# Optimization experiments

Hardware: AMD Instinct MI355X
Metric: run time of the kernel (lower is better)

Reference implementation:

```python
import jax, jax.numpy as jnp
import numpy as np

HIDDEN = 1024
HEADS = 16
HEAD_SIZE = HIDDEN // HEADS
N, L = 2, 2048


def setup_inputs() -> dict:
    key = jax.random.key(0)
    ks = jax.random.split(key, 9)
    s = 1.0 / np.sqrt(HIDDEN)
    x = jax.random.normal(ks[0], (N, L, HIDDEN), dtype=jnp.float32)
    Wq = jax.random.normal(ks[1], (HIDDEN, HIDDEN), dtype=jnp.float32) * s
    Wk = jax.random.normal(ks[2], (HIDDEN, HIDDEN), dtype=jnp.float32) * s
    Wv = jax.random.normal(ks[3], (HIDDEN, HIDDEN), dtype=jnp.float32) * s
    Wo = jax.random.normal(ks[4], (HIDDEN, HIDDEN), dtype=jnp.float32) * s
    bq = jax.random.normal(ks[5], (HIDDEN,), dtype=jnp.float32) * s
    bk = jax.random.normal(ks[6], (HIDDEN,), dtype=jnp.float32) * s
    bv = jax.random.normal(ks[7], (HIDDEN,), dtype=jnp.float32) * s
    bo = jax.random.normal(ks[8], (HIDDEN,), dtype=jnp.float32) * s
    return {"x": x, "Wq": Wq, "bq": bq, "Wk": Wk, "bk": bk,
            "Wv": Wv, "bv": bv, "Wo": Wo, "bo": bo}


def reference(x, Wq, bq, Wk, bk, Wv, bv, Wo, bo):
    n, l, _ = x.shape
    # torch Linear: y = x @ W.T + b
    q = (x @ Wq.T + bq).reshape(n, l, HEADS, HEAD_SIZE)
    k = (x @ Wk.T + bk).reshape(n, l, HEADS, HEAD_SIZE)
    v = (x @ Wv.T + bv).reshape(n, l, HEADS, HEAD_SIZE)
    # NOTE: module does NOT apply 1/sqrt(head_size) scaling
    sims = jnp.einsum('nqhs,nkhs->nhqk', q, k)  # (N,H,L,L)
    attn = jax.nn.softmax(sims, axis=-1)
    ctx = jnp.einsum('nhqk,nkhs->nqhs', attn, v).reshape(n, l, HIDDEN)
    return ctx @ Wo.T + bo
```

## Files before the change

### kernel.cpp

```cpp
#include <hip/hip_runtime.h>
#include <stdint.h>
#include <stddef.h>

#define HIDDEN 1024
#define HEADS  16
#define HDIM   64
#define NBATCH 2
#define SEQ    2048
#define TOK    (NBATCH*SEQ)

typedef __attribute__((ext_vector_type(8))) short bf16x8;
typedef __attribute__((ext_vector_type(4))) float f32x4;
typedef unsigned short bf16u;

__device__ __forceinline__ unsigned short f2bf(float f) {
  union { float f; unsigned int u; } c; c.f = f;
  unsigned int u = c.u;
  unsigned int r = (u + 0x7fffu + ((u >> 16) & 1u)) >> 16;
  return (unsigned short)r;
}

__global__ __launch_bounds__(256) void convert_kernel(
    const float* __restrict__ x,
    const float* __restrict__ wq, const float* __restrict__ wk,
    const float* __restrict__ wv, const float* __restrict__ wo,
    bf16u* __restrict__ xb, bf16u* __restrict__ wqkvb, bf16u* __restrict__ wob) {
  const int XG = TOK*HIDDEN/4;
  const int WG = HIDDEN*HIDDEN/4;
  int i = blockIdx.x*blockDim.x + threadIdx.x;
  const float* src; bf16u* dst; int off;
  if (i < XG)            { src = x;  dst = xb;                      off = i; }
  else if (i < XG+WG)    { src = wq; dst = wqkvb;                   off = i-XG; }
  else if (i < XG+2*WG)  { src = wk; dst = wqkvb +   HIDDEN*HIDDEN; off = i-XG-WG; }
  else if (i < XG+3*WG)  { src = wv; dst = wqkvb + 2*HIDDEN*HIDDEN; off = i-XG-2*WG; }
  else if (i < XG+4*WG)  { src = wo; dst = wob;                     off = i-XG-3*WG; }
  else return;
  float4 v = ((const float4*)src)[off];
  ushort4 o;
  o.x = f2bf(v.x); o.y = f2bf(v.y); o.z = f2bf(v.z); o.w = f2bf(v.w);
  *(ushort4*)&dst[(size_t)off*4] = o;
}

__device__ __forceinline__ void gemm_core(const bf16u* __restrict__ Abase,
                                          const bf16u* __restrict__ Bbase,
                                          bf16u* As, bf16u* Bs,
                                          f32x4 (&acc)[4][4]) {
  const int K = HIDDEN;
  const int t = threadIdx.x;
  const int w = t >> 6, lane = t & 63;
  const int wm = (w >> 1) * 64, wn = (w & 1) * 64;
  const int row = lane & 15, kq = (lane >> 4) * 8;
  const int c0 = t, c1 = t + 256;
  const int rA0 = c0 >> 2, k80 = (c0 & 3) * 8;
  const int rA1 = c1 >> 2, k81 = (c1 & 3) * 8;
  bf16u* ldsA0 = As + (size_t)(w*64)*8;
  bf16u* ldsA1 = As + (size_t)(256 + w*64)*8;
  bf16u* ldsB0 = Bs + (size_t)(w*64)*8;
  bf16u* ldsB1 = Bs + (size_t)(256 + w*64)*8;

  for (int k0 = 0; k0 < K; k0 += 32) {
    __builtin_amdgcn_global_load_lds(
        (const __attribute__((address_space(1))) void*)(Abase + (size_t)rA0*K + k0 + k80),
        (__attribute__((address_space(3))) void*)ldsA0, 16, 0, 0);
    __builtin_amdgcn_global_load_lds(
        (const __attribute__((address_space(1))) void*)(Abase + (size_t)rA1*K + k0 + k81),
        (__attribute__((address_space(3))) void*)ldsA1, 16, 0, 0);
    __builtin_amdgcn_global_load_lds(
        (const __attribute__((address_space(1))) void*)(Bbase + (size_t)rA0*K + k0 + k80),
        (__attribute__((address_space(3))) void*)ldsB0, 16, 0, 0);
    __builtin_amdgcn_global_load_lds(
        (const __attribute__((address_space(1))) void*)(Bbase + (size_t)rA1*K + k0 + k81),
        (__attribute__((address_space(3))) void*)ldsB1, 16, 0, 0);
    __syncthreads();
    bf16x8 af[4], bf[4];
    #pragma unroll
    for (int mi = 0; mi < 4; mi++)
      af[mi] = *(const bf16x8*)&As[(wm + mi*16 + row)*32 + kq];
    #pragma unroll
    for (int ni = 0; ni < 4; ni++)
      bf[ni] = *(const bf16x8*)&Bs[(wn + ni*16 + row)*32 + kq];
    #pragma unroll
    for (int mi = 0; mi < 4; mi++)
      #pragma unroll
      for (int ni = 0; ni < 4; ni++)
        acc[mi][ni] = __builtin_amdgcn_mfma_f32_16x16x32_bf16(af[mi], bf[ni], acc[mi][ni], 0, 0, 0);
    __syncthreads();
  }
}

__global__ __launch_bounds__(256) void qkv_kernel(
    const bf16u* __restrict__ xb, const bf16u* __restrict__ wqkvb,
    const float* __restrict__ bq, const float* __restrict__ bk, const float* __restrict__ bv,
    bf16u* __restrict__ qb, bf16u* __restrict__ kb, bf16u* __restrict__ vtb) {
  __shared__ bf16u As[128*32];
  __shared__ bf16u Bs[128*32];
  f32x4 z = {0.f,0.f,0.f,0.f};
  f32x4 acc[4][4];
  #pragma unroll
  for (int i = 0; i < 4; i++)
    #pragma unroll
    for (int j = 0; j < 4; j++) acc[i][j] = z;
  const int n0 = blockIdx.x * 128, m0 = blockIdx.y * 128;
  gemm_core(xb + (size_t)m0*HIDDEN, wqkvb + (size_t)n0*HIDDEN, As, Bs, acc);

  const int t = threadIdx.x, w = t >> 6, lane = t & 63;
  const int wm = (w >> 1) * 64, wn = (w & 1) * 64;
  #pragma unroll
  for (int mi = 0; mi < 4; mi++) {
    #pragma unroll
    for (int ni = 0; ni < 4; ni++) {
      const int col = n0 + wn + ni*16 + (lane & 15);
      const int which = col >> 10, c = col & 1023;
      const int head = c >> 6, d = c & 63;
      const float bias = (which == 0 ? bq : (which == 1 ? bk : bv))[c];
      #pragma unroll
      for (int j = 0; j < 4; j++) {
        const int rowm = m0 + wm + mi*16 + ((lane >> 4) * 4) + j;
        const int n = rowm >> 11, l = rowm & 2047;
        const bf16u hv = f2bf(acc[mi][ni][j] + bias);
        if (which == 0)
          qb[(((size_t)n*HEADS + head)*SEQ + l)*HDIM + d] = hv;
        else if (which == 1)
          kb[(((size_t)n*HEADS + head)*SEQ + l)*HDIM + d] = hv;
        else
          vtb[(((size_t)n*HEADS + head)*HDIM + d)*SEQ + l] = hv;
      }
    }
  }
}

__global__ __launch_bounds__(256) void attn_kernel(
    const bf16u* __restrict__ qb, const bf16u* __restrict__ kb,
    const bf16u* __restrict__ vtb, bf16u* __restrict__ ctxb) {
  __shared__ bf16u Ks[2][64*64];
  __shared__ bf16u Vs[2][64*64];
  __shared__ bf16u Pl[4][16*64];
  const int t = threadIdx.x, w = t >> 6, lane = t & 63;
  const int row = lane & 15, hi = lane >> 4, kq8 = hi * 8;
  const int qt = blockIdx.x, nh = blockIdx.y;
  const int n = nh >> 4, h = nh & 15;
  const bf16u* Qb = qb  + (size_t)nh * SEQ * HDIM;
  const bf16u* Kb = kb  + (size_t)nh * SEQ * HDIM;
  const bf16u* Vt = vtb + (size_t)nh * HDIM * SEQ;

  const int c0 = w*64 + lane, c1 = c0 + 256;
  const int r0 = c0 >> 3, e0 = ((c0 & 7) ^ (r0 & 7)) * 8;
  const int r1 = c1 >> 3, e1 = ((c1 & 7) ^ (r1 & 7)) * 8;

  const int qrow = qt*64 + w*16 + row;
  const bf16x8 aq0 = *(const bf16x8*)&Qb[(size_t)qrow*HDIM + kq8];
  const bf16x8 aq1 = *(const bf16x8*)&Qb[(size_t)qrow*HDIM + 32 + kq8];
  f32x4 z = {0.f,0.f,0.f,0.f};
  float mr[4] = {-1e30f,-1e30f,-1e30f,-1e30f};
  float lr[4] = {0.f,0.f,0.f,0.f};
  f32x4 ao[4] = {z,z,z,z};
  bf16u* P = &Pl[w][0];

  auto stage = [&](int buf, int kv0) {
    __builtin_amdgcn_global_load_lds(
        (const __attribute__((address_space(1))) void*)(Kb + (size_t)(kv0 + r0)*HDIM + e0),
        (__attribute__((address_space(3))) void*)(&Ks[buf][(size_t)(w*64)*8]), 16, 0, 0);
    __builtin_amdgcn_global_load_lds(
        (const __attribute__((address_space(1))) void*)(Kb + (size_t)(kv0 + r1)*HDIM + e1),
        (__attribute__((address_space(3))) void*)(&Ks[buf][(size_t)(256 + w*64)*8]), 16, 0, 0);
    __builtin_amdgcn_global_load_lds(
        (const __attribute__((address_space(1))) void*)(Vt + (size_t)r0*SEQ + kv0 + e0),
        (__attribute__((address_space(3))) void*)(&Vs[buf][(size_t)(w*64)*8]), 16, 0, 0);
    __builtin_amdgcn_global_load_lds(
        (const __attribute__((address_space(1))) void*)(Vt + (size_t)r1*SEQ + kv0 + e1),
        (__attribute__((address_space(3))) void*)(&Vs[buf][(size_t)(256 + w*64)*8]), 16, 0, 0);
  };

  stage(0, 0);
  asm volatile("s_waitcnt vmcnt(0)" ::: "memory");
  __builtin_amdgcn_s_barrier();

  for (int it = 0; it < 32; ++it) {
    const int cur = it & 1;
    if (it < 31) stage(cur ^ 1, (it + 1) * 64);

    f32x4 s[4] = {z,z,z,z};
    bf16x8 bk0[4], bk1[4];
    #pragma unroll
    for (int cb = 0; cb < 4; cb++) {
      const int kvr = cb*16 + row;
      const int sw = kvr & 7;
      bk0[cb] = *(const bf16x8*)&Ks[cur][kvr*64 + ((hi     ^ sw) * 8)];
      bk1[cb] = *(const bf16x8*)&Ks[cur][kvr*64 + (((4+hi) ^ sw) * 8)];
    }
    __builtin_amdgcn_s_setprio(1);
    #pragma unroll
    for (int cb = 0; cb < 4; cb++) {
      s[cb] = __builtin_amdgcn_mfma_f32_16x16x32_bf16(aq0, bk0[cb], s[cb], 0, 0, 0);
      s[cb] = __builtin_amdgcn_mfma_f32_16x16x32_bf16(aq1, bk1[cb], s[cb], 0, 0, 0);
    }
    __builtin_amdgcn_s_setprio(0);

    float tmax[4], rs[4], sc[4], p[4][4];
    #pragma unroll
    for (int j = 0; j < 4; j++)
      tmax[j] = fmaxf(fmaxf(s[0][j], s[1][j]), fmaxf(s[2][j], s[3][j]));
    #pragma unroll
    for (int m = 1; m <= 8; m <<= 1)
      #pragma unroll
      for (int j = 0; j < 4; j++)
        tmax[j] = fmaxf(tmax[j], __shfl_xor(tmax[j], m));
    #pragma unroll
    for (int j = 0; j < 4; j++) {
      float nm = fmaxf(mr[j], tmax[j]);
      sc[j] = __expf(mr[j] - nm);
      mr[j] = nm;
      rs[j] = 0.f;
    }
    #pragma unroll
    for (int cb = 0; cb < 4; cb++)
      #pragma unroll
      for (int j = 0; j < 4; j++) {
        p[cb][j] = __expf(s[cb][j] - mr[j]);
        rs[j] += p[cb][j];
      }
    #pragma unroll
    for (int m = 1; m <= 8; m <<= 1)
      #pragma unroll
      for (int j = 0; j < 4; j++)
        rs[j] += __shfl_xor(rs[j], m);
    #pragma unroll
    for (int j = 0; j < 4; j++)
      lr[j] = lr[j]*sc[j] + rs[j];
    #pragma unroll
    for (int db = 0; db < 4; db++)
      #pragma unroll
      for (int j = 0; j < 4; j++)
        ao[db][j] *= sc[j];

    #pragma unroll
    for (int cb = 0; cb < 4; cb++)
      #pragma unroll
      for (int j = 0; j < 4; j++) {
        const int qr = hi*4 + j;
        P[qr*64 + (((cb*16 + row) ^ ((qr & 7) << 3)))] = f2bf(p[cb][j]);
      }
    asm volatile("s_waitcnt lgkmcnt(0)" ::: "memory");
    __builtin_amdgcn_sched_barrier(0);

    bf16x8 ap[2], bv[2][4];
    #pragma unroll
    for (int ks = 0; ks < 2; ks++) {
      ap[ks] = *(const bf16x8*)&P[row*64 + (((ks*4+hi) ^ (row & 7)) * 8)];
      #pragma unroll
      for (int db = 0; db < 4; db++) {
        const int dr = db*16 + row;
        bv[ks][db] = *(const bf16x8*)&Vs[cur][dr*64 + (((ks*4+hi) ^ (dr & 7)) * 8)];
      }
    }
    __builtin_amdgcn_s_setprio(1);
    #pragma unroll
    for (int ks = 0; ks < 2; ks++)
      #pragma unroll
      for (int db = 0; db < 4; db++)
        ao[db] = __builtin_amdgcn_mfma_f32_16x16x32_bf16(ap[ks], bv[ks][db], ao[db], 0, 0, 0);
    __builtin_amdgcn_s_setprio(0);

    if (it < 31) asm volatile("s_waitcnt vmcnt(0)" ::: "memory");
    __builtin_amdgcn_s_barrier();
  }

  float inv[4];
  #pragma unroll
  for (int j = 0; j < 4; j++) inv[j] = 1.0f / lr[j];
  #pragma unroll
  for (int db = 0; db < 4; db++)
    #pragma unroll
    for (int j = 0; j < 4; j++) {
      const int l = qt*64 + w*16 + (lane >> 4)*4 + j;
      const int d = db*16 + row;
      ctxb[((size_t)n*SEQ + l)*HIDDEN + h*HDIM + d] = f2bf(ao[db][j] * inv[j]);
    }
}

__global__ __launch_bounds__(256) void oproj_kernel(
    const bf16u* __restrict__ ctxb, const bf16u* __restrict__ wob,
    const float* __restrict__ bo, float* __restrict__ out) {
  __shared__ bf16u As[128*32];
  __shared__ bf16u Bs[128*32];
  f32x4 z = {0.f,0.f,0.f,0.f};
  f32x4 acc[4][4];
  #pragma unroll
  for (int i = 0; i < 4; i++)
    #pragma unroll
    for (int j = 0; j < 4; j++) acc[i][j] = z;
  const int n0 = blockIdx.x * 128, m0 = blockIdx.y * 128;
  gemm_core(ctxb + (size_t)m0*HIDDEN, wob + (size_t)n0*HIDDEN, As, Bs, acc);

  const int t = threadIdx.x, w = t >> 6, lane = t & 63;
  const int wm = (w >> 1) * 64, wn = (w & 1) * 64;
  #pragma unroll
  for (int mi = 0; mi < 4; mi++) {
    #pragma unroll
    for (int ni = 0; ni < 4; ni++) {
      const int col = n0 + wn + ni*16 + (lane & 15);
      const float bias = bo[col];
      #pragma unroll
      for (int j = 0; j < 4; j++) {
        const int rowm = m0 + wm + mi*16 + ((lane >> 4)*4) + j;
        out[(size_t)rowm*HIDDEN + col] = acc[mi][ni][j] + bias;
      }
    }
  }
}

extern "C" void kernel_launch(void* const* d_in, const int* in_sizes, int n_in,
                              void* d_out, int out_size, void* d_ws, size_t ws_size,
                              hipStream_t stream) {
  const float* x  = (const float*)d_in[0];
  const float* Wq = (const float*)d_in[1];
  const float* bq = (const float*)d_in[2];
  const float* Wk = (const float*)d_in[3];
  const float* bk = (const float*)d_in[4];
  const float* Wv = (const float*)d_in[5];
  const float* bv = (const float*)d_in[6];
  const float* Wo = (const float*)d_in[7];
  const float* bo = (const float*)d_in[8];
  float* out = (float*)d_out;

  bf16u* xb    = (bf16u*)d_ws;
  bf16u* wqkvb = xb    + (size_t)TOK*HIDDEN;
  bf16u* wob   = wqkvb + (size_t)3*HIDDEN*HIDDEN;
  bf16u* qb    = wob   + (size_t)HIDDEN*HIDDEN;
  bf16u* kb    = qb    + (size_t)TOK*HIDDEN;
  bf16u* vtb   = kb    + (size_t)TOK*HIDDEN;
  bf16u* ctxb  = vtb   + (size_t)TOK*HIDDEN;

  convert_kernel<<<8192, 256, 0, stream>>>(x, Wq, Wk, Wv, Wo, xb, wqkvb, wob);
  qkv_kernel<<<dim3(24, 32), 256, 0, stream>>>(xb, wqkvb, bq, bk, bv, qb, kb, vtb);
  attn_kernel<<<dim3(32, 32), 256, 0, stream>>>(qb, kb, vtb, ctxb);
  oproj_kernel<<<dim3(8, 32), 256, 0, stream>>>(ctxb, wob, bo, out);
}
```

Before: 277.8 us.

## Transpose QK^T MFMA so each lane owns one query row; skip rescale when max unchanged

Swaps the MFMA operands so the score tile comes out transposed, with each lane holding one query row. The row max and row sum then need only two cross-lane shuffles instead of four per value, and the softmax state shrinks to a scalar per lane. Rescaling of the output accumulator is skipped when no row max rises across the wave, and P is written to LDS as packed 8-byte bf16 stores using the library conversion. The gains come from fewer shuffles and LDS stores, at the cost of a divergent branch and extra shuffles to redistribute the scale factors to the output layout.

Measured after the change: 246.3 us. -11.3%, faster.

```diff
diff --git a/kernel.cpp b/kernel.cpp
--- a/kernel.cpp
+++ b/kernel.cpp
@@ -1,4 +1,5 @@
 #include <hip/hip_runtime.h>
+#include <hip/hip_bf16.h>
 #include <stdint.h>
 #include <stddef.h>
 
@@ -18,6 +19,14 @@
   unsigned int u = c.u;
   unsigned int r = (u + 0x7fffu + ((u >> 16) & 1u)) >> 16;
   return (unsigned short)r;
+}
+
+__device__ __forceinline__ unsigned int pk2bf(float a, float b) {
+  __hip_bfloat16 ba = __float2bfloat16(a), bb = __float2bfloat16(b);
+  unsigned short ua, ub;
+  __builtin_memcpy(&ua, &ba, 2);
+  __builtin_memcpy(&ub, &bb, 2);
+  return (unsigned int)ua | ((unsigned int)ub << 16);
 }
 
 __global__ __launch_bounds__(256) void convert_kernel(
@@ -151,8 +160,8 @@
   const bf16x8 aq0 = *(const bf16x8*)&Qb[(size_t)qrow*HDIM + kq8];
   const bf16x8 aq1 = *(const bf16x8*)&Qb[(size_t)qrow*HDIM + 32 + kq8];
   f32x4 z = {0.f,0.f,0.f,0.f};
-  float mr[4] = {-1e30f,-1e30f,-1e30f,-1e30f};
-  float lr[4] = {0.f,0.f,0.f,0.f};
+  float mr = -1e30f;
+  float lr = 0.f;
   f32x4 ao[4] = {z,z,z,z};
   bf16u* P = &Pl[w][0];
 
@@ -179,7 +188,7 @@
     const int cur = it & 1;
     if (it < 31) stage(cur ^ 1, (it + 1) * 64);
 
-    f32x4 s[4] = {z,z,z,z};
+    f32x4 s[4];
     bf16x8 bk0[4], bk1[4];
     #pragma unroll
     for (int cb = 0; cb < 4; cb++) {
@@ -191,55 +200,57 @@
     __builtin_amdgcn_s_setprio(1);
     #pragma unroll
     for (int cb = 0; cb < 4; cb++) {
-      s[cb] = __builtin_amdgcn_mfma_f32_16x16x32_bf16(aq0, bk0[cb], s[cb], 0, 0, 0);
-      s[cb] = __builtin_amdgcn_mfma_f32_16x16x32_bf16(aq1, bk1[cb], s[cb], 0, 0, 0);
+      s[cb] = __builtin_amdgcn_mfma_f32_16x16x32_bf16(bk0[cb], aq0, z, 0, 0, 0);
+      s[cb] = __builtin_amdgcn_mfma_f32_16x16x32_bf16(bk1[cb], aq1, s[cb], 0, 0, 0);
     }
     __builtin_amdgcn_s_setprio(0);
 
-    float tmax[4], rs[4], sc[4], p[4][4];
-    #pragma unroll
-    for (int j = 0; j < 4; j++)
-      tmax[j] = fmaxf(fmaxf(s[0][j], s[1][j]), fmaxf(s[2][j], s[3][j]));
-    #pragma unroll
-    for (int m = 1; m <= 8; m <<= 1)
+    float pm = s[0][0];
+    #pragma unroll
+    for (int cb = 0; cb < 4; cb++)
       #pragma unroll
       for (int j = 0; j < 4; j++)
-        tmax[j] = fmaxf(tmax[j], __shfl_xor(tmax[j], m));
-    #pragma unroll
-    for (int j = 0; j < 4; j++) {
-      float nm = fmaxf(mr[j], tmax[j]);
-      sc[j] = __expf(mr[j] - nm);
-      mr[j] = nm;
-      rs[j] = 0.f;
-    }
+        pm = fmaxf(pm, s[cb][j]);
+    pm = fmaxf(pm, __shfl_xor(pm, 16));
+    pm = fmaxf(pm, __shfl_xor(pm, 32));
+
+    if (!__all(pm <= mr)) {
+      const float nm = fmaxf(mr, pm);
+      const float sc = __expf(mr - nm);
+      mr = nm;
+      lr *= sc;
+      float scj[4];
+      #pragma unroll
+      for (int j = 0; j < 4; j++)
+        scj[j] = __shfl(sc, hi*4 + j);
+      #pragma unroll
+      for (int db = 0; db < 4; db++)
+        #pragma unroll
+        for (int j = 0; j < 4; j++)
+          ao[db][j] *= scj[j];
+    }
+
+    float p[4][4];
+    float rs = 0.f;
     #pragma unroll
     for (int cb = 0; cb < 4; cb++)
       #pragma unroll
       for (int j = 0; j < 4; j++) {
-        p[cb][j] = __expf(s[cb][j] - mr[j]);
-        rs[j] += p[cb][j];
+        p[cb][j] = __expf(s[cb][j] - mr);
+        rs += p[cb][j];
       }
-    #pragma unroll
-    for (int m = 1; m <= 8; m <<= 1)
-      #pragma unroll
-      for (int j = 0; j < 4; j++)
-        rs[j] += __shfl_xor(rs[j], m);
-    #pragma unroll
-    for (int j = 0; j < 4; j++)
-      lr[j] = lr[j]*sc[j] + rs[j];
-    #pragma unroll
-    for (int db = 0; db < 4; db++)
-      #pragma unroll
-      for (int j = 0; j < 4; j++)
-        ao[db][j] *= sc[j];
-
-    #pragma unroll
-    for (int cb = 0; cb < 4; cb++)
-      #pragma unroll
-      for (int j = 0; j < 4; j++) {
-        const int qr = hi*4 + j;
-        P[qr*64 + (((cb*16 + row) ^ ((qr & 7) << 3)))] = f2bf(p[cb][j]);
-      }
+    rs += __shfl_xor(rs, 16);
+    rs += __shfl_xor(rs, 32);
+    lr += rs;
+
+    #pragma unroll
+    for (int cb = 0; cb < 4; cb++) {
+      uint2 pk;
+      pk.x = pk2bf(p[cb][0], p[cb][1]);
+      pk.y = pk2bf(p[cb][2], p[cb][3]);
+      const int slot = cb*2 + (hi >> 1);
+      *(uint2*)&P[row*64 + ((slot ^ (row & 7)) * 8) + (hi & 1)*4] = pk;
+    }
     asm volatile("s_waitcnt lgkmcnt(0)" ::: "memory");
     __builtin_amdgcn_sched_barrier(0);
 
@@ -265,16 +276,18 @@
     __builtin_amdgcn_s_barrier();
   }
 
-  float inv[4];
-  #pragma unroll
-  for (int j = 0; j < 4; j++) inv[j] = 1.0f / lr[j];
+  const float linv = 1.0f / lr;
+  float invj[4];
+  #pragma unroll
+  for (int j = 0; j < 4; j++)
+    invj[j] = __shfl(linv, hi*4 + j);
   #pragma unroll
   for (int db = 0; db < 4; db++)
     #pragma unroll
     for (int j = 0; j < 4; j++) {
-      const int l = qt*64 + w*16 + (lane >> 4)*4 + j;
+      const int l = qt*64 + w*16 + hi*4 + j;
       const int d = db*16 + row;
-      ctxb[((size_t)n*SEQ + l)*HIDDEN + h*HDIM + d] = f2bf(ao[db][j] * inv[j]);
+      ctxb[((size_t)n*SEQ + l)*HIDDEN + h*HDIM + d] = f2bf(ao[db][j] * invj[j]);
     }
 }
 
```
